# Optimization experiments

Hardware: AMD Instinct MI355X
Metric: run time of the kernel (lower is better)

The kernel has to match this reference:

```python
import jax, jax.numpy as jnp
import numpy as np

DIM = 1024
NUM_HEADS = 16
HEAD_DIM = DIM // NUM_HEADS
SCALE = HEAD_DIM ** -0.5


def setup_inputs() -> dict:
    key = jax.random.key(0)
    ks = jax.random.split(key, 5)
    B, N, C = 2, 2048, DIM
    x = jax.random.normal(ks[0], (B, N, C), dtype=jnp.float32)
    s = 1.0 / np.sqrt(C)
    W_qkv = jax.random.normal(ks[1], (C, 3 * C), dtype=jnp.float32) * s
    b_qkv = jax.random.normal(ks[2], (3 * C,), dtype=jnp.float32) * 0.01
    W_proj = jax.random.normal(ks[3], (C, C), dtype=jnp.float32) * s
    b_proj = jax.random.normal(ks[4], (C,), dtype=jnp.float32) * 0.01
    return {"x": x, "W_qkv": W_qkv, "b_qkv": b_qkv, "W_proj": W_proj, "b_proj": b_proj}


def reference(x, W_qkv, b_qkv, W_proj, b_proj):
    B, N, C = x.shape
    qkv = x @ W_qkv + b_qkv                      # [B, N, 3C]
    qkv = qkv.reshape(B, N, 3, NUM_HEADS, HEAD_DIM)
    qkv = jnp.transpose(qkv, (2, 0, 3, 1, 4))    # [3, B, H, N, hd]
    # Faithful to source quirk: q = k = v = qkv[2]
    v = qkv[2]
    q = v
    k = v
    attn = jnp.einsum('bhnd,bhmd->bhnm', q, k) * SCALE
    attn = jax.nn.softmax(attn, axis=-1)
    out = jnp.einsum('bhnm,bhmd->bhnd', attn, v)  # [B, H, N, hd]
    out = jnp.transpose(out, (0, 2, 1, 3)).reshape(B, N, C)
    return out @ W_proj + b_proj
```

## Files before the change

kernel.cpp:

```cpp
#include <hip/hip_runtime.h>

typedef __bf16    bf16x4 __attribute__((ext_vector_type(4)));
typedef __bf16    bf16x8 __attribute__((ext_vector_type(8)));
typedef _Float16  f16x2  __attribute__((ext_vector_type(2)));
typedef _Float16  f16x4  __attribute__((ext_vector_type(4)));
typedef _Float16  f16x8  __attribute__((ext_vector_type(8)));
typedef float     f32x4  __attribute__((ext_vector_type(4)));

#define MFMA16x16x32 __builtin_amdgcn_mfma_f32_16x16x32_bf16
#define MFMA16x16x16F __builtin_amdgcn_mfma_f32_16x16x16f16

__device__ __forceinline__ void gload_lds16(const void* g, void* l) {
  __builtin_amdgcn_global_load_lds((const __attribute__((address_space(1))) void*)g,
                                   (__attribute__((address_space(3))) void*)l, 16, 0, 0);
}

__device__ __forceinline__ f16x2 pkrtz(float a, float b) {
  return __builtin_bit_cast(f16x2, __builtin_amdgcn_cvt_pkrtz(a, b));
}

__global__ __launch_bounds__(256) void xcast(const float* __restrict__ x,
                                             __bf16* __restrict__ xb) {
  const int gid = blockIdx.x * 256 + threadIdx.x;
  float4 v = ((const float4*)x)[gid];
  bf16x4 o;
  o.x = (__bf16)v.x; o.y = (__bf16)v.y; o.z = (__bf16)v.z; o.w = (__bf16)v.w;
  *(bf16x4*)&xb[(size_t)gid * 4] = o;
}

__global__ __launch_bounds__(256) void prep_transpose(const float* __restrict__ Wqkv,
                                                      const float* __restrict__ Wproj,
                                                      __bf16* __restrict__ WvT,
                                                      __bf16* __restrict__ WpT) {
  __shared__ float tile[64][65];
  const float* src; __bf16* dst; int ld, c0;
  if (blockIdx.z == 0) { src = Wqkv; dst = WvT; ld = 3072; c0 = 2048; }
  else                 { src = Wproj; dst = WpT; ld = 1024; c0 = 0; }
  const int k0 = blockIdx.x * 64, n0 = blockIdx.y * 64;
  const int t = threadIdx.x;
#pragma unroll
  for (int i = 0; i < 4; i++) {
    int idx = t + i * 256; int r = idx >> 4, g = idx & 15;
    float4 v = *(const float4*)&src[(size_t)(k0 + r) * ld + c0 + n0 + g * 4];
    tile[r][g * 4 + 0] = v.x; tile[r][g * 4 + 1] = v.y;
    tile[r][g * 4 + 2] = v.z; tile[r][g * 4 + 3] = v.w;
  }
  __syncthreads();
#pragma unroll
  for (int i = 0; i < 4; i++) {
    int idx = t + i * 256; int n = idx >> 4, g = idx & 15;
    bf16x4 o;
    o.x = (__bf16)tile[g * 4 + 0][n]; o.y = (__bf16)tile[g * 4 + 1][n];
    o.z = (__bf16)tile[g * 4 + 2][n]; o.w = (__bf16)tile[g * 4 + 3][n];
    *(bf16x4*)&dst[(size_t)(n0 + n) * 1024 + k0 + g * 4] = o;
  }
}

__global__ __launch_bounds__(256, 2) void gemm_v(const __bf16* __restrict__ xb,
                                                 const __bf16* __restrict__ WvT,
                                                 const float* __restrict__ bias,
                                                 __bf16* __restrict__ V,
                                                 _Float16* __restrict__ Vt) {
  constexpr int K = 1024;
  __shared__ char lds[2 * 12288];
  const int t = threadIdx.x, w = t >> 6, l = t & 63, lr = l & 15, quad = l >> 4;
  const int wr = w >> 1, wc = w & 1;
  const int m0 = blockIdx.x * 128, n0 = blockIdx.y * 64;

  const int rA = t >> 2, kg = t & 3;
  const __bf16* pA0 = xb + (size_t)(m0 + rA) * K + kg * 8;
  const __bf16* pA1 = pA0 + (size_t)64 * K;
  const __bf16* pB  = WvT + (size_t)(n0 + rA) * K + kg * 8;

  f32x4 acc[4][2] = {};
  {
    char* buf = (char*)lds;
    gload_lds16(pA0, buf + t * 16);
    gload_lds16(pA1, buf + 4096 + t * 16);
    gload_lds16(pB,  buf + 8192 + t * 16);
  }
  for (int it = 0; it < 32; ++it) {
    __syncthreads();
    if (it + 1 < 32) {
      pA0 += 32; pA1 += 32; pB += 32;
      char* buf = (char*)lds + ((it + 1) & 1) * 12288;
      gload_lds16(pA0, buf + t * 16);
      gload_lds16(pA1, buf + 4096 + t * 16);
      gload_lds16(pB,  buf + 8192 + t * 16);
    }
    const char* Abuf = (const char*)lds + (it & 1) * 12288;
    const char* Bbuf = Abuf + 8192;
    bf16x8 af[4], bv[2];
#pragma unroll
    for (int mi = 0; mi < 4; mi++)
      af[mi] = *(const bf16x8*)(Abuf + (wr * 64 + mi * 16 + lr) * 64 + quad * 16);
#pragma unroll
    for (int nc = 0; nc < 2; nc++)
      bv[nc] = *(const bf16x8*)(Bbuf + (wc * 32 + nc * 16 + lr) * 64 + quad * 16);
#pragma unroll
    for (int mi = 0; mi < 4; mi++)
#pragma unroll
      for (int nc = 0; nc < 2; nc++)
        acc[mi][nc] = MFMA16x16x32(af[mi], bv[nc], acc[mi][nc], 0, 0, 0);
  }
  const int by = blockIdx.y;
#pragma unroll
  for (int mi = 0; mi < 4; mi++) {
    const int grow0 = m0 + wr * 64 + mi * 16 + quad * 4;
    const int b_ = grow0 >> 11, tok0 = grow0 & 2047;
#pragma unroll
    for (int nc = 0; nc < 2; nc++) {
      const int d = wc * 32 + nc * 16 + lr;
      const int gcol = n0 + d;
      float bb = bias[gcol];
      float v0 = acc[mi][nc][0] + bb, v1 = acc[mi][nc][1] + bb;
      float v2 = acc[mi][nc][2] + bb, v3 = acc[mi][nc][3] + bb;
      V[(size_t)(grow0 + 0) * 1024 + gcol] = (__bf16)v0;
      V[(size_t)(grow0 + 1) * 1024 + gcol] = (__bf16)v1;
      V[(size_t)(grow0 + 2) * 1024 + gcol] = (__bf16)v2;
      V[(size_t)(grow0 + 3) * 1024 + gcol] = (__bf16)v3;
      f16x2 lo = pkrtz(v0, v1), hi = pkrtz(v2, v3);
      f16x4 pv; pv[0] = lo[0]; pv[1] = lo[1]; pv[2] = hi[0]; pv[3] = hi[1];
      *(f16x4*)&Vt[((size_t)(b_ * 16 + by) * 64 + d) * 2048 + tok0] = pv;
    }
  }
}

__global__ __launch_bounds__(256, 2) void gemm_proj(const __bf16* __restrict__ A,
                                                    const __bf16* __restrict__ Bt,
                                                    const float* __restrict__ bias,
                                                    float* __restrict__ outp) {
  constexpr int K = 1024, Nn = 1024;
  __shared__ char lds[2 * 12288];
  const int t = threadIdx.x, w = t >> 6, l = t & 63, lr = l & 15, quad = l >> 4;
  const int wr = w >> 1, wc = w & 1;
  const int m0 = blockIdx.x * 128, n0 = blockIdx.y * 64;

  const int rA = t >> 2, kg = t & 3;
  const __bf16* pA0 = A + (size_t)(m0 + rA) * K + kg * 8;
  const __bf16* pA1 = pA0 + (size_t)64 * K;
  const __bf16* pB  = Bt + (size_t)(n0 + rA) * K + kg * 8;

  f32x4 acc[4][2] = {};
  {
    char* buf = (char*)lds;
    gload_lds16(pA0, buf + t * 16);
    gload_lds16(pA1, buf + 4096 + t * 16);
    gload_lds16(pB,  buf + 8192 + t * 16);
  }
  for (int it = 0; it < 32; ++it) {
    __syncthreads();
    if (it + 1 < 32) {
      pA0 += 32; pA1 += 32; pB += 32;
      char* buf = (char*)lds + ((it + 1) & 1) * 12288;
      gload_lds16(pA0, buf + t * 16);
      gload_lds16(pA1, buf + 4096 + t * 16);
      gload_lds16(pB,  buf + 8192 + t * 16);
    }
    const char* Abuf = (const char*)lds + (it & 1) * 12288;
    const char* Bbuf = Abuf + 8192;
    bf16x8 af[4], bv[2];
#pragma unroll
    for (int mi = 0; mi < 4; mi++)
      af[mi] = *(const bf16x8*)(Abuf + (wr * 64 + mi * 16 + lr) * 64 + quad * 16);
#pragma unroll
    for (int nc = 0; nc < 2; nc++)
      bv[nc] = *(const bf16x8*)(Bbuf + (wc * 32 + nc * 16 + lr) * 64 + quad * 16);
#pragma unroll
    for (int mi = 0; mi < 4; mi++)
#pragma unroll
      for (int nc = 0; nc < 2; nc++)
        acc[mi][nc] = MFMA16x16x32(af[mi], bv[nc], acc[mi][nc], 0, 0, 0);
  }
#pragma unroll
  for (int mi = 0; mi < 4; mi++) {
    const int grow0 = m0 + wr * 64 + mi * 16 + quad * 4;
#pragma unroll
    for (int nc = 0; nc < 2; nc++) {
      const int gcol = n0 + wc * 32 + nc * 16 + lr;
      float bb = bias[gcol];
#pragma unroll
      for (int r = 0; r < 4; r++)
        outp[(size_t)(grow0 + r) * Nn + gcol] = acc[mi][nc][r] + bb;
    }
  }
}

__global__ __launch_bounds__(512, 4) void attn_kernel(const __bf16* __restrict__ V,
                                                      const _Float16* __restrict__ Vt,
                                                      __bf16* __restrict__ O) {
  __shared__ char lds[65536];
  const int t = threadIdx.x, w = t >> 6, l = t & 63, lr = l & 15, quad = l >> 4;
  const int bh = blockIdx.x, b = bh >> 4, h = bh & 15;
  const int qb = blockIdx.y * 128 + (w & 3) * 16;
  const int part = w >> 2;

  const __bf16* Vbh = V + (size_t)b * 2048 * 1024 + h * 64;
  const _Float16* Vtbh = Vt + (size_t)bh * 64 * 2048;

  bf16x8 qf[2][2];
#pragma unroll
  for (int sub = 0; sub < 2; sub++)
#pragma unroll
    for (int ks = 0; ks < 2; ks++)
      qf[sub][ks] = *(const bf16x8*)(Vbh + (size_t)(qb + sub * 64 + lr) * 1024 + ks * 32 + quad * 8);

  const int kva = t >> 3, ua = (t & 7) ^ (kva & 7);
  const __bf16* pK0 = Vbh + (size_t)kva * 1024 + ua * 8;
  const __bf16* pK1 = pK0 + (size_t)64 * 1024;
  const int kb_ = t >> 7, d_ = (t >> 1) & 63, qh = (t & 1) ^ ((d_ >> 2) & 1);
  const _Float16* pV0 = Vtbh + (size_t)d_ * 2048 + kb_ * 16 + qh * 8;
  const _Float16* pV1 = pV0 + 64;

  const int koff0 = lr * 128 + ((quad ^ (lr & 7)) * 16);
  const int koff1 = lr * 128 + (((4 + quad) ^ (lr & 7)) * 16);
  const int xq = (quad >> 1) ^ ((lr >> 2) & 1);
  const int voff = lr * 32 + xq * 16 + (quad & 1) * 8;

  f32x4 o[2][4] = {};
  f32x4 l5[2] = {};
  f16x4 ones; ones[0] = ones[1] = ones[2] = ones[3] = (_Float16)1.0f;
  const float Cc = 0.18033688011112042f;
  const float C8 = 11.541560327111707f;

  {
    char* base = lds;
    gload_lds16(pK0, base + t * 16);
    gload_lds16(pV0, base + 8192 + t * 16);
    gload_lds16(pK1, base + 16384 + t * 16);
    gload_lds16(pV1, base + 24576 + t * 16);
  }
  for (int it = 0; it < 16; ++it) {
    __syncthreads();
    if (it + 1 < 16) {
      pK0 += 131072; pK1 += 131072; pV0 += 128; pV1 += 128;
      char* base = lds + ((it + 1) & 1) * 32768;
      gload_lds16(pK0, base + t * 16);
      gload_lds16(pV0, base + 8192 + t * 16);
      gload_lds16(pK1, base + 16384 + t * 16);
      gload_lds16(pV1, base + 24576 + t * 16);
    }
    const char* Kb = lds + (it & 1) * 32768 + part * 16384;
    const char* Vb = Kb + 8192;

    f32x4 s[2][4] = {};
#pragma unroll
    for (int ks = 0; ks < 2; ks++) {
      const int ko = ks ? koff1 : koff0;
#pragma unroll
      for (int rb = 0; rb < 4; rb++) {
        bf16x8 kf = *(const bf16x8*)(Kb + ko + rb * 2048);
        s[0][rb] = MFMA16x16x32(kf, qf[0][ks], s[0][rb], 0, 0, 0);
        s[1][rb] = MFMA16x16x32(kf, qf[1][ks], s[1][rb], 0, 0, 0);
      }
    }

    f16x4 pf[2][4];
#pragma unroll
    for (int sub = 0; sub < 2; sub++)
#pragma unroll
      for (int rb = 0; rb < 4; rb++) {
        float p0 = __builtin_amdgcn_exp2f(s[sub][rb][0] * Cc - C8);
        float p1 = __builtin_amdgcn_exp2f(s[sub][rb][1] * Cc - C8);
        float p2 = __builtin_amdgcn_exp2f(s[sub][rb][2] * Cc - C8);
        float p3 = __builtin_amdgcn_exp2f(s[sub][rb][3] * Cc - C8);
        f16x2 lo = pkrtz(p0, p1);
        f16x2 hi = pkrtz(p2, p3);
        pf[sub][rb][0] = lo[0]; pf[sub][rb][1] = lo[1];
        pf[sub][rb][2] = hi[0]; pf[sub][rb][3] = hi[1];
      }

#pragma unroll
    for (int kb = 0; kb < 4; kb++) {
#pragma unroll
      for (int db = 0; db < 4; db++) {
        f16x4 vf = *(const f16x4*)(Vb + voff + db * 512 + kb * 2048);
        o[0][db] = MFMA16x16x16F(pf[0][kb], vf, o[0][db], 0, 0, 0);
        o[1][db] = MFMA16x16x16F(pf[1][kb], vf, o[1][db], 0, 0, 0);
      }
      l5[0] = MFMA16x16x16F(pf[0][kb], ones, l5[0], 0, 0, 0);
      l5[1] = MFMA16x16x16F(pf[1][kb], ones, l5[1], 0, 0, 0);
    }
  }

  __syncthreads();
  float* xch = (float*)lds;
  if (w >= 4) {
    float* dsto = xch + (w - 4) * 2048;
#pragma unroll
    for (int sub = 0; sub < 2; sub++)
#pragma unroll
      for (int db = 0; db < 4; db++)
        *(f32x4*)&dsto[(sub * 4 + db) * 256 + l * 4] = o[sub][db];
    float* dstl = xch + 8192 + (w - 4) * 512;
    *(f32x4*)&dstl[l * 4] = l5[0];
    *(f32x4*)&dstl[256 + l * 4] = l5[1];
  }
  __syncthreads();
  if (w < 4) {
    const float* srco = xch + w * 2048;
    const float* srcl = xch + 8192 + w * 512;
#pragma unroll
    for (int sub = 0; sub < 2; sub++) {
#pragma unroll
      for (int db = 0; db < 4; db++)
        o[sub][db] += *(const f32x4*)&srco[(sub * 4 + db) * 256 + l * 4];
      l5[sub] += *(const f32x4*)&srcl[sub * 256 + l * 4];
    }
#pragma unroll
    for (int sub = 0; sub < 2; sub++)
#pragma unroll
      for (int r = 0; r < 4; r++) {
        float lv = 1.0f / l5[sub][r];
        int token = b * 2048 + qb + sub * 64 + quad * 4 + r;
#pragma unroll
        for (int db = 0; db < 4; db++)
          O[(size_t)token * 1024 + h * 64 + db * 16 + lr] = (__bf16)(o[sub][db][r] * lv);
      }
  }
}

extern "C" void kernel_launch(void* const* d_in, const int* in_sizes, int n_in,
                              void* d_out, int out_size, void* d_ws, size_t ws_size,
                              hipStream_t stream) {
  (void)in_sizes; (void)n_in; (void)out_size; (void)ws_size;
  const float* x     = (const float*)d_in[0];
  const float* Wqkv  = (const float*)d_in[1];
  const float* bqkv  = (const float*)d_in[2];
  const float* Wproj = (const float*)d_in[3];
  const float* bproj = (const float*)d_in[4];

  char* ws = (char*)d_ws;
  __bf16*    V   = (__bf16*)(ws);
  _Float16*  Vt  = (_Float16*)(ws + (size_t)8  * 1048576);
  __bf16*    Ob  = (__bf16*)(ws + (size_t)16 * 1048576);
  __bf16*    xb  = (__bf16*)(ws + (size_t)16 * 1048576);
  __bf16*    WvT = (__bf16*)(ws + (size_t)24 * 1048576);
  __bf16*    WpT = (__bf16*)(ws + (size_t)26 * 1048576);

  xcast<<<dim3(4096), 256, 0, stream>>>(x, xb);
  prep_transpose<<<dim3(16, 16, 2), 256, 0, stream>>>(Wqkv, Wproj, WvT, WpT);
  gemm_v<<<dim3(32, 16), 256, 0, stream>>>(xb, WvT, bqkv + 2048, V, Vt);
  attn_kernel<<<dim3(32, 16), 512, 0, stream>>>(V, Vt, Ob);
  gemm_proj<<<dim3(32, 16), 256, 0, stream>>>(Ob, WpT, bproj, (float*)d_out);
}
```

Measured before the change: 162.5 us.

## Double GEMM K-tile depth to 64 and XOR-swizzle LDS layout in both GEMMs

Both the V-projection and output-projection GEMMs now stage a 64-wide K slice per iteration instead of 32, halving the loop trip count and the number of barriers. The LDS layout is XOR-swizzled on 16-byte chunks, applied on the global-to-LDS load side and on the fragment read offsets, to avoid bank conflicts with the wider 128-byte rows. Fragment offsets are precomputed outside the loop. LDS use per block doubles to 48KB, which may limit occupancy alongside the 2-block launch bound.

```diff
diff --git a/kernel.cpp b/kernel.cpp
--- a/kernel.cpp
+++ b/kernel.cpp
@@ -62,46 +62,69 @@
                                                  __bf16* __restrict__ V,
                                                  _Float16* __restrict__ Vt) {
   constexpr int K = 1024;
-  __shared__ char lds[2 * 12288];
+  __shared__ char lds[2 * 24576];
   const int t = threadIdx.x, w = t >> 6, l = t & 63, lr = l & 15, quad = l >> 4;
   const int wr = w >> 1, wc = w & 1;
   const int m0 = blockIdx.x * 128, n0 = blockIdx.y * 64;
 
-  const int rA = t >> 2, kg = t & 3;
-  const __bf16* pA0 = xb + (size_t)(m0 + rA) * K + kg * 8;
-  const __bf16* pA1 = pA0 + (size_t)64 * K;
-  const __bf16* pB  = WvT + (size_t)(n0 + rA) * K + kg * 8;
+  const int row0 = t >> 3;
+  const int scol = (t & 7) ^ (row0 & 7);
+  const __bf16* pA = xb  + (size_t)(m0 + row0) * K + scol * 8;
+  const __bf16* pB = WvT + (size_t)(n0 + row0) * K + scol * 8;
 
   f32x4 acc[4][2] = {};
   {
     char* buf = (char*)lds;
-    gload_lds16(pA0, buf + t * 16);
-    gload_lds16(pA1, buf + 4096 + t * 16);
-    gload_lds16(pB,  buf + 8192 + t * 16);
-  }
-  for (int it = 0; it < 32; ++it) {
+    gload_lds16(pA,          buf + t * 16);
+    gload_lds16(pA + 32 * K, buf + 4096  + t * 16);
+    gload_lds16(pA + 64 * K, buf + 8192  + t * 16);
+    gload_lds16(pA + 96 * K, buf + 12288 + t * 16);
+    gload_lds16(pB,          buf + 16384 + t * 16);
+    gload_lds16(pB + 32 * K, buf + 20480 + t * 16);
+  }
+  int aoff[4][2], boff[2][2];
+#pragma unroll
+  for (int mi = 0; mi < 4; mi++)
+#pragma unroll
+    for (int ks = 0; ks < 2; ks++)
+      aoff[mi][ks] = (wr * 64 + mi * 16 + lr) * 128 + (((ks * 4 + quad) ^ (lr & 7)) * 16);
+#pragma unroll
+  for (int nc = 0; nc < 2; nc++)
+#pragma unroll
+    for (int ks = 0; ks < 2; ks++)
+      boff[nc][ks] = 16384 + (wc * 32 + nc * 16 + lr) * 128 + (((ks * 4 + quad) ^ (lr & 7)) * 16);
+
+  for (int it = 0; it < 16; ++it) {
     __syncthreads();
-    if (it + 1 < 32) {
-      pA0 += 32; pA1 += 32; pB += 32;
-      char* buf = (char*)lds + ((it + 1) & 1) * 12288;
-      gload_lds16(pA0, buf + t * 16);
-      gload_lds16(pA1, buf + 4096 + t * 16);
-      gload_lds16(pB,  buf + 8192 + t * 16);
-    }
-    const char* Abuf = (const char*)lds + (it & 1) * 12288;
-    const char* Bbuf = Abuf + 8192;
-    bf16x8 af[4], bv[2];
+    if (it + 1 < 16) {
+      pA += 64; pB += 64;
+      char* buf = (char*)lds + ((it + 1) & 1) * 24576;
+      gload_lds16(pA,          buf + t * 16);
+      gload_lds16(pA + 32 * K, buf + 4096  + t * 16);
+      gload_lds16(pA + 64 * K, buf + 8192  + t * 16);
+      gload_lds16(pA + 96 * K, buf + 12288 + t * 16);
+      gload_lds16(pB,          buf + 16384 + t * 16);
+      gload_lds16(pB + 32 * K, buf + 20480 + t * 16);
+    }
+    const char* buf = (const char*)lds + (it & 1) * 24576;
+    bf16x8 af[4][2], bv[2][2];
 #pragma unroll
     for (int mi = 0; mi < 4; mi++)
-      af[mi] = *(const bf16x8*)(Abuf + (wr * 64 + mi * 16 + lr) * 64 + quad * 16);
+#pragma unroll
+      for (int ks = 0; ks < 2; ks++)
+        af[mi][ks] = *(const bf16x8*)(buf + aoff[mi][ks]);
 #pragma unroll
     for (int nc = 0; nc < 2; nc++)
-      bv[nc] = *(const bf16x8*)(Bbuf + (wc * 32 + nc * 16 + lr) * 64 + quad * 16);
+#pragma unroll
+      for (int ks = 0; ks < 2; ks++)
+        bv[nc][ks] = *(const bf16x8*)(buf + boff[nc][ks]);
 #pragma unroll
     for (int mi = 0; mi < 4; mi++)
 #pragma unroll
       for (int nc = 0; nc < 2; nc++)
-        acc[mi][nc] = MFMA16x16x32(af[mi], bv[nc], acc[mi][nc], 0, 0, 0);
+#pragma unroll
+        for (int ks = 0; ks < 2; ks++)
+          acc[mi][nc] = MFMA16x16x32(af[mi][ks], bv[nc][ks], acc[mi][nc], 0, 0, 0);
   }
   const int by = blockIdx.y;
 #pragma unroll
@@ -131,46 +154,69 @@
                                                     const float* __restrict__ bias,
                                                     float* __restrict__ outp) {
   constexpr int K = 1024, Nn = 1024;
-  __shared__ char lds[2 * 12288];
+  __shared__ char lds[2 * 24576];
   const int t = threadIdx.x, w = t >> 6, l = t & 63, lr = l & 15, quad = l >> 4;
   const int wr = w >> 1, wc = w & 1;
   const int m0 = blockIdx.x * 128, n0 = blockIdx.y * 64;
 
-  const int rA = t >> 2, kg = t & 3;
-  const __bf16* pA0 = A + (size_t)(m0 + rA) * K + kg * 8;
-  const __bf16* pA1 = pA0 + (size_t)64 * K;
-  const __bf16* pB  = Bt + (size_t)(n0 + rA) * K + kg * 8;
+  const int row0 = t >> 3;
+  const int scol = (t & 7) ^ (row0 & 7);
+  const __bf16* pA = A  + (size_t)(m0 + row0) * K + scol * 8;
+  const __bf16* pB = Bt + (size_t)(n0 + row0) * K + scol * 8;
 
   f32x4 acc[4][2] = {};
   {
     char* buf = (char*)lds;
-    gload_lds16(pA0, buf + t * 16);
-    gload_lds16(pA1, buf + 4096 + t * 16);
-    gload_lds16(pB,  buf + 8192 + t * 16);
-  }
-  for (int it = 0; it < 32; ++it) {
+    gload_lds16(pA,          buf + t * 16);
+    gload_lds16(pA + 32 * K, buf + 4096  + t * 16);
+    gload_lds16(pA + 64 * K, buf + 8192  + t * 16);
+    gload_lds16(pA + 96 * K, buf + 12288 + t * 16);
+    gload_lds16(pB,          buf + 16384 + t * 16);
+    gload_lds16(pB + 32 * K, buf + 20480 + t * 16);
+  }
+  int aoff[4][2], boff[2][2];
+#pragma unroll
+  for (int mi = 0; mi < 4; mi++)
+#pragma unroll
+    for (int ks = 0; ks < 2; ks++)
+      aoff[mi][ks] = (wr * 64 + mi * 16 + lr) * 128 + (((ks * 4 + quad) ^ (lr & 7)) * 16);
+#pragma unroll
+  for (int nc = 0; nc < 2; nc++)
+#pragma unroll
+    for (int ks = 0; ks < 2; ks++)
+      boff[nc][ks] = 16384 + (wc * 32 + nc * 16 + lr) * 128 + (((ks * 4 + quad) ^ (lr & 7)) * 16);
+
+  for (int it = 0; it < 16; ++it) {
     __syncthreads();
-    if (it + 1 < 32) {
-      pA0 += 32; pA1 += 32; pB += 32;
-      char* buf = (char*)lds + ((it + 1) & 1) * 12288;
-      gload_lds16(pA0, buf + t * 16);
-      gload_lds16(pA1, buf + 4096 + t * 16);
-      gload_lds16(pB,  buf + 8192 + t * 16);
-    }
-    const char* Abuf = (const char*)lds + (it & 1) * 12288;
-    const char* Bbuf = Abuf + 8192;
-    bf16x8 af[4], bv[2];
+    if (it + 1 < 16) {
+      pA += 64; pB += 64;
+      char* buf = (char*)lds + ((it + 1) & 1) * 24576;
+      gload_lds16(pA,          buf + t * 16);
+      gload_lds16(pA + 32 * K, buf + 4096  + t * 16);
+      gload_lds16(pA + 64 * K, buf + 8192  + t * 16);
+      gload_lds16(pA + 96 * K, buf + 12288 + t * 16);
+      gload_lds16(pB,          buf + 16384 + t * 16);
+      gload_lds16(pB + 32 * K, buf + 20480 + t * 16);
+    }
+    const char* buf = (const char*)lds + (it & 1) * 24576;
+    bf16x8 af[4][2], bv[2][2];
 #pragma unroll
     for (int mi = 0; mi < 4; mi++)
-      af[mi] = *(const bf16x8*)(Abuf + (wr * 64 + mi * 16 + lr) * 64 + quad * 16);
+#pragma unroll
+      for (int ks = 0; ks < 2; ks++)
+        af[mi][ks] = *(const bf16x8*)(buf + aoff[mi][ks]);
 #pragma unroll
     for (int nc = 0; nc < 2; nc++)
-      bv[nc] = *(const bf16x8*)(Bbuf + (wc * 32 + nc * 16 + lr) * 64 + quad * 16);
+#pragma unroll
+      for (int ks = 0; ks < 2; ks++)
+        bv[nc][ks] = *(const bf16x8*)(buf + boff[nc][ks]);
 #pragma unroll
     for (int mi = 0; mi < 4; mi++)
 #pragma unroll
       for (int nc = 0; nc < 2; nc++)
-        acc[mi][nc] = MFMA16x16x32(af[mi], bv[nc], acc[mi][nc], 0, 0, 0);
+#pragma unroll
+        for (int ks = 0; ks < 2; ks++)
+          acc[mi][nc] = MFMA16x16x32(af[mi][ks], bv[nc][ks], acc[mi][nc], 0, 0, 0);
   }
 #pragma unroll
   for (int mi = 0; mi < 4; mi++) {
```

Result: faster. 154.0 us (-5.3%).
